# Optimization experiments

Measured on AMD Instinct MI355X. Metric: run time of the kernel, lower is better.

The kernel has to match this reference:

```python
import jax, jax.numpy as jnp
import numpy as np

N = 4096

def setup_inputs() -> dict:
    key = jax.random.key(0)
    kA, kB = jax.random.split(key)
    # A and B are upper-triangular inputs, as the module assumes
    A = jnp.triu(jax.random.normal(kA, (N, N), dtype=jnp.float32))
    B = jnp.triu(jax.random.normal(kB, (N, N), dtype=jnp.float32))
    return {"A": A, "B": B}

def reference(A, B):
    # C = triu(A @ B); product of upper-triangular matrices is upper-triangular,
    # the kernel additionally masks the lower triangle of the output.
    return jnp.triu(A @ B)
```

## Files before the change

kernel.cpp:

```cpp
#include <hip/hip_runtime.h>


#define N    4096
#define NB   32
#define BM   128
#define PK   64
#define NWG  1024
#define CH   12
#define MAXF 1280
#define MAXL 64

typedef __attribute__((ext_vector_type(8))) __bf16 bf16x8;
typedef __attribute__((ext_vector_type(4))) float  floatx4;
typedef __attribute__((ext_vector_type(8))) unsigned short ushort8;

struct Sched {
    unsigned short wgoff[NWG + 1];
    unsigned int   chunks[MAXF];
    int nf;
};

constexpr Sched make_sched() {
    Sched s{};
    unsigned int fr_sz[MAXF] = {};
    unsigned int fr_pk[MAXF] = {};
    int nf = 0;
    for (int d = NB - 1; d >= 0; --d) {
        const int npj  = 2 * (d + 1);
        const int nc   = (npj + CH - 1) / CH;
        const int base = npj / nc, rem = npj % nc;
        for (int bi = 0; bi + d < NB; ++bi) {
            const int bj = bi + d;
            int p0 = 0;
            for (int c = 0; c < nc; ++c) {
                const int fnp = base + (c < rem ? 1 : 0);
                fr_sz[nf] = (unsigned)fnp;
                fr_pk[nf] = (unsigned)bi | ((unsigned)bj << 5) |
                            ((unsigned)p0 << 10) | ((unsigned)fnp << 17) |
                            ((nc > 1 ? 1u : 0u) << 24);
                ++nf;
                p0 += fnp;
            }
        }
    }
    int order[MAXF] = {};
    int pos = 0;
    for (int sz = CH; sz >= 1; --sz)
        for (int i = 0; i < nf; ++i)
            if ((int)fr_sz[i] == sz) order[pos++] = i;
    int bcnt[MAXL] = {};
    int blist[MAXL][NWG] = {};
    for (int b = 0; b < NWG; ++b) blist[0][b] = NWG - 1 - b;
    bcnt[0] = NWG;
    int assign[MAXF] = {};
    int minload = 0;
    for (int k = 0; k < nf; ++k) {
        const int f = order[k];
        while (bcnt[minload] == 0) ++minload;
        const int b  = blist[minload][--bcnt[minload]];
        const int nl = minload + (int)fr_sz[f];
        blist[nl][bcnt[nl]++] = b;
        assign[f] = b;
    }
    int cnt[NWG] = {};
    for (int f = 0; f < nf; ++f) cnt[assign[f]]++;
    s.wgoff[0] = 0;
    for (int b = 0; b < NWG; ++b)
        s.wgoff[b + 1] = (unsigned short)(s.wgoff[b] + cnt[b]);
    int fill[NWG] = {};
    for (int f = 0; f < nf; ++f) {
        const int b = assign[f];
        s.chunks[s.wgoff[b] + fill[b]++] = fr_pk[f];
    }
    s.nf = nf;
    return s;
}

__device__ constexpr Sched g_sched = make_sched();

__device__ __forceinline__ unsigned short f32_to_bf16_rne(float f) {
    unsigned u = __builtin_bit_cast(unsigned, f);
    unsigned r = u + 0x7fffu + ((u >> 16) & 1u);
    return (unsigned short)(r >> 16);
}

__device__ __forceinline__ void gload_lds16(const unsigned short* g,
                                            unsigned short* l) {
    __builtin_amdgcn_global_load_lds(
        (const __attribute__((address_space(1))) void*)g,
        (__attribute__((address_space(3))) void*)l, 16, 0, 0);
}

__global__ __launch_bounds__(256)
void prep_kernel(const float* __restrict__ A, const float* __restrict__ B,
                 unsigned short* __restrict__ Ab, unsigned short* __restrict__ Bt,
                 float* __restrict__ C) {
    __shared__ float tile[64][65];
    const int bx = blockIdx.x, by = blockIdx.y;
    const int x0 = bx * 64, y0 = by * 64;
    const int xb = bx >> 1, yb = by >> 1;
    const int t  = threadIdx.x;
    const int tr = t >> 2, tc = (t & 3) * 16;

    if (xb >= yb) {
        const float* src = A + (size_t)(y0 + tr) * N + x0 + tc;
        const float4 v0 = ((const float4*)src)[0];
        const float4 v1 = ((const float4*)src)[1];
        const float4 v2 = ((const float4*)src)[2];
        const float4 v3 = ((const float4*)src)[3];
        ushort8 o0, o1;
        o0[0]=f32_to_bf16_rne(v0.x); o0[1]=f32_to_bf16_rne(v0.y);
        o0[2]=f32_to_bf16_rne(v0.z); o0[3]=f32_to_bf16_rne(v0.w);
        o0[4]=f32_to_bf16_rne(v1.x); o0[5]=f32_to_bf16_rne(v1.y);
        o0[6]=f32_to_bf16_rne(v1.z); o0[7]=f32_to_bf16_rne(v1.w);
        o1[0]=f32_to_bf16_rne(v2.x); o1[1]=f32_to_bf16_rne(v2.y);
        o1[2]=f32_to_bf16_rne(v2.z); o1[3]=f32_to_bf16_rne(v2.w);
        o1[4]=f32_to_bf16_rne(v3.x); o1[5]=f32_to_bf16_rne(v3.y);
        o1[6]=f32_to_bf16_rne(v3.z); o1[7]=f32_to_bf16_rne(v3.w);
        unsigned short* dst = Ab + (size_t)(y0 + tr) * N + x0 + tc;
        ((ushort8*)dst)[0] = o0;
        ((ushort8*)dst)[1] = o1;
    }
    if (xb <= yb) {
        const float* src = B + (size_t)(x0 + tr) * N + y0 + tc;
        const float4 v0 = ((const float4*)src)[0];
        const float4 v1 = ((const float4*)src)[1];
        const float4 v2 = ((const float4*)src)[2];
        const float4 v3 = ((const float4*)src)[3];
        float* d = &tile[tr][tc];
        d[0]=v0.x; d[1]=v0.y; d[2]=v0.z; d[3]=v0.w;
        d[4]=v1.x; d[5]=v1.y; d[6]=v1.z; d[7]=v1.w;
        d[8]=v2.x; d[9]=v2.y; d[10]=v2.z; d[11]=v2.w;
        d[12]=v3.x; d[13]=v3.y; d[14]=v3.z; d[15]=v3.w;
        __syncthreads();
        ushort8 o0, o1;
        #pragma unroll
        for (int i = 0; i < 8; ++i) o0[i] = f32_to_bf16_rne(tile[tc + i][tr]);
        #pragma unroll
        for (int i = 0; i < 8; ++i) o1[i] = f32_to_bf16_rne(tile[tc + 8 + i][tr]);
        unsigned short* dst = Bt + (size_t)(y0 + tr) * N + x0 + tc;
        ((ushort8*)dst)[0] = o0;
        ((ushort8*)dst)[1] = o1;
    }
    if (xb < yb || (xb - yb) >= 6) {
        float4 z = {0.f, 0.f, 0.f, 0.f};
        float* dst = C + (size_t)(y0 + tr) * N + x0 + tc;
        ((float4*)dst)[0] = z; ((float4*)dst)[1] = z;
        ((float4*)dst)[2] = z; ((float4*)dst)[3] = z;
    }
}

__global__ __launch_bounds__(256, 4)
void trimm_kernel(const unsigned short* __restrict__ Ab,
                  const unsigned short* __restrict__ Bt,
                  float* __restrict__ C) {
    __shared__ unsigned short sA[BM * PK];
    __shared__ unsigned short sB[BM * PK];

    const int tid  = threadIdx.x;
    const int w    = tid >> 6;
    const int lane = tid & 63;
    const int quad = lane >> 4;
    const int l15  = lane & 15;

    const int m0 = (w >> 1) * 64;
    const int n0 = (w & 1) * 64;

    const int srow   = lane >> 3;
    const int schunk = ((lane & 7) ^ srow) * 8;
    int rr[4];
    unsigned short* dA[4];
    unsigned short* dB[4];
    #pragma unroll
    for (int i = 0; i < 4; ++i) {
        rr[i] = w * 32 + i * 8 + srow;
        dA[i] = sA + (w * 32 + i * 8) * PK;
        dB[i] = sB + (w * 32 + i * 8) * PK;
    }

    const int e  = l15 & 7;
    const int c0 = ((quad ^ (e & 3)) + 4 * (e >> 2)) * 8;
    const int c1 = ((quad ^ (e & 3)) + 4 * (1 ^ (e >> 2))) * 8;

    const int b  = (int)blockIdx.x;
    const int j0 = g_sched.wgoff[b];
    const int j1 = g_sched.wgoff[b + 1];

    for (int j = j0; j < j1; ++j) {
        const unsigned int ck = g_sched.chunks[j];
        const int bi   = ck & 31;
        const int bj   = (ck >> 5) & 31;
        const int p0   = (ck >> 10) & 127;
        const int cnp  = (ck >> 17) & 127;
        const bool is_at = (ck >> 24) & 1u;

        const int row0 = bi * BM;
        const int col0 = bj * BM;
        const int k0   = bi * BM + p0 * PK;

        floatx4 acc[4][4] = {};

        const unsigned short* gA[4];
        const unsigned short* gB[4];
        #pragma unroll
        for (int i = 0; i < 4; ++i) {
            gA[i] = Ab + (size_t)(row0 + rr[i]) * N + k0 + schunk;
            gB[i] = Bt + (size_t)(col0 + rr[i]) * N + k0 + schunk;
        }

        for (int ph = 0; ph < cnp; ++ph) {
            #pragma unroll
            for (int i = 0; i < 4; ++i) { gload_lds16(gA[i], dA[i]); gA[i] += PK; }
            #pragma unroll
            for (int i = 0; i < 4; ++i) { gload_lds16(gB[i], dB[i]); gB[i] += PK; }
            __syncthreads();
            #pragma unroll
            for (int h = 0; h < 2; ++h) {
                const int ch = h ? c1 : c0;
                bf16x8 af[4], bfr[4];
                #pragma unroll
                for (int t = 0; t < 4; ++t) {
                    af[t]  = *(const bf16x8*)&sA[(m0 + t * 16 + l15) * PK + ch];
                    bfr[t] = *(const bf16x8*)&sB[(n0 + t * 16 + l15) * PK + ch];
                }
                #pragma unroll
                for (int tm = 0; tm < 4; ++tm)
                    #pragma unroll
                    for (int tn = 0; tn < 4; ++tn)
                        acc[tm][tn] = __builtin_amdgcn_mfma_f32_16x16x32_bf16(
                            af[tm], bfr[tn], acc[tm][tn], 0, 0, 0);
            }
            __syncthreads();
        }

        #pragma unroll
        for (int tm = 0; tm < 4; ++tm) {
            const int grow_base = row0 + m0 + tm * 16 + quad * 4;
            #pragma unroll
            for (int tn = 0; tn < 4; ++tn) {
                const int gcol = col0 + n0 + tn * 16 + l15;
                #pragma unroll
                for (int r = 0; r < 4; ++r) {
                    const int grow = grow_base + r;
                    const float v = acc[tm][tn][r];
                    if (is_at) {
                        atomicAdd(&C[(size_t)grow * N + gcol], v);
                    } else if (bi != bj) {
                        C[(size_t)grow * N + gcol] = v;
                    } else {
                        C[(size_t)grow * N + gcol] = (gcol >= grow) ? v : 0.0f;
                    }
                }
            }
        }
    }
}

extern "C" void kernel_launch(void* const* d_in, const int* in_sizes, int n_in,
                              void* d_out, int out_size, void* d_ws, size_t ws_size,
                              hipStream_t stream) {
    const float* A = (const float*)d_in[0];
    const float* B = (const float*)d_in[1];
    float* C = (float*)d_out;

    unsigned short* Ab = (unsigned short*)d_ws;
    unsigned short* Bt = Ab + (size_t)N * N;

    prep_kernel<<<dim3(N / 64, N / 64), dim3(256), 0, stream>>>(A, B, Ab, Bt, C);
    trimm_kernel<<<dim3(NWG), dim3(256), 0, stream>>>(Ab, Bt, C);
}
```

Before: 249.0 us.

## Double-buffer LDS tiles and halve workgroup count with larger chunks

Adds a two-stage LDS ping-pong so the global-to-LDS loads for the next K panel are issued before the MFMAs on the current panel run, removing one barrier per step. To fit the doubled shared memory, occupancy is lowered to 2 blocks per SIMD group. The persistent schedule is also changed to 512 workgroups with chunks of up to 24 panels, so atomic splitting happens on fewer, longer chunks, and the band in which C is pre-zeroed is widened to match. The cost is lower occupancy and fewer workgroups, which may leave some CUs idle or unbalanced.

```diff
diff --git a/kernel.cpp b/kernel.cpp
--- a/kernel.cpp
+++ b/kernel.cpp
@@ -5,9 +5,9 @@
 #define NB   32
 #define BM   128
 #define PK   64
-#define NWG  1024
-#define CH   12
-#define MAXF 1280
+#define NWG  512
+#define CH   24
+#define MAXF 832
 #define MAXL 64
 
 typedef __attribute__((ext_vector_type(8))) __bf16 bf16x8;
@@ -142,7 +142,7 @@
         ((ushort8*)dst)[0] = o0;
         ((ushort8*)dst)[1] = o1;
     }
-    if (xb < yb || (xb - yb) >= 6) {
+    if (xb < yb || (xb - yb) >= 12) {
         float4 z = {0.f, 0.f, 0.f, 0.f};
         float* dst = C + (size_t)(y0 + tr) * N + x0 + tc;
         ((float4*)dst)[0] = z; ((float4*)dst)[1] = z;
@@ -150,12 +150,12 @@
     }
 }
 
-__global__ __launch_bounds__(256, 4)
+__global__ __launch_bounds__(256, 2)
 void trimm_kernel(const unsigned short* __restrict__ Ab,
                   const unsigned short* __restrict__ Bt,
                   float* __restrict__ C) {
-    __shared__ unsigned short sA[BM * PK];
-    __shared__ unsigned short sB[BM * PK];
+    __shared__ unsigned short sA[2][BM * PK];
+    __shared__ unsigned short sB[2][BM * PK];
 
     const int tid  = threadIdx.x;
     const int w    = tid >> 6;
@@ -168,14 +168,11 @@
 
     const int srow   = lane >> 3;
     const int schunk = ((lane & 7) ^ srow) * 8;
-    int rr[4];
-    unsigned short* dA[4];
-    unsigned short* dB[4];
+    int rr[4], ldso[4];
     #pragma unroll
     for (int i = 0; i < 4; ++i) {
-        rr[i] = w * 32 + i * 8 + srow;
-        dA[i] = sA + (w * 32 + i * 8) * PK;
-        dB[i] = sB + (w * 32 + i * 8) * PK;
+        rr[i]   = w * 32 + i * 8 + srow;
+        ldso[i] = (w * 32 + i * 8) * PK;
     }
 
     const int e  = l15 & 7;
@@ -185,6 +182,8 @@
     const int b  = (int)blockIdx.x;
     const int j0 = g_sched.wgoff[b];
     const int j1 = g_sched.wgoff[b + 1];
+
+    int cur = 0;
 
     for (int j = j0; j < j1; ++j) {
         const unsigned int ck = g_sched.chunks[j];
@@ -208,20 +207,27 @@
             gB[i] = Bt + (size_t)(col0 + rr[i]) * N + k0 + schunk;
         }
 
-        for (int ph = 0; ph < cnp; ++ph) {
-            #pragma unroll
-            for (int i = 0; i < 4; ++i) { gload_lds16(gA[i], dA[i]); gA[i] += PK; }
-            #pragma unroll
-            for (int i = 0; i < 4; ++i) { gload_lds16(gB[i], dB[i]); gB[i] += PK; }
-            __syncthreads();
+        cur ^= 1;
+        #pragma unroll
+        for (int i = 0; i < 4; ++i) { gload_lds16(gA[i], &sA[cur][ldso[i]]); gA[i] += PK; }
+        #pragma unroll
+        for (int i = 0; i < 4; ++i) { gload_lds16(gB[i], &sB[cur][ldso[i]]); gB[i] += PK; }
+        __syncthreads();
+
+        for (int ph = 0; ph < cnp - 1; ++ph) {
+            const int nxt = cur ^ 1;
+            #pragma unroll
+            for (int i = 0; i < 4; ++i) { gload_lds16(gA[i], &sA[nxt][ldso[i]]); gA[i] += PK; }
+            #pragma unroll
+            for (int i = 0; i < 4; ++i) { gload_lds16(gB[i], &sB[nxt][ldso[i]]); gB[i] += PK; }
             #pragma unroll
             for (int h = 0; h < 2; ++h) {
                 const int ch = h ? c1 : c0;
                 bf16x8 af[4], bfr[4];
                 #pragma unroll
                 for (int t = 0; t < 4; ++t) {
-                    af[t]  = *(const bf16x8*)&sA[(m0 + t * 16 + l15) * PK + ch];
-                    bfr[t] = *(const bf16x8*)&sB[(n0 + t * 16 + l15) * PK + ch];
+                    af[t]  = *(const bf16x8*)&sA[cur][(m0 + t * 16 + l15) * PK + ch];
+                    bfr[t] = *(const bf16x8*)&sB[cur][(n0 + t * 16 + l15) * PK + ch];
                 }
                 #pragma unroll
                 for (int tm = 0; tm < 4; ++tm)
@@ -231,6 +237,25 @@
                             af[tm], bfr[tn], acc[tm][tn], 0, 0, 0);
             }
             __syncthreads();
+            cur = nxt;
+        }
+        {
+            #pragma unroll
+            for (int h = 0; h < 2; ++h) {
+                const int ch = h ? c1 : c0;
+                bf16x8 af[4], bfr[4];
+                #pragma unroll
+                for (int t = 0; t < 4; ++t) {
+                    af[t]  = *(const bf16x8*)&sA[cur][(m0 + t * 16 + l15) * PK + ch];
+                    bfr[t] = *(const bf16x8*)&sB[cur][(n0 + t * 16 + l15) * PK + ch];
+                }
+                #pragma unroll
+                for (int tm = 0; tm < 4; ++tm)
+                    #pragma unroll
+                    for (int tn = 0; tn < 4; ++tn)
+                        acc[tm][tn] = __builtin_amdgcn_mfma_f32_16x16x32_bf16(
+                            af[tm], bfr[tn], acc[tm][tn], 0, 0, 0);
+            }
         }
 
         #pragma unroll
```

Result: faster. 219.0 us (-12.1%).

## Software-pipeline triangular GEMM with register prefetch and double-buffered LDS across chunks

Applied to the files above, without the earlier changes.

Replaces the direct global-to-LDS loads with a register-staged prefetch that runs two k-phases ahead, continuing across chunk boundaries, into double-buffered LDS. This drops one barrier per phase and hides global latency behind MFMA work. Workgroups are halved to 512 with larger chunks (CH 24), and the zeroing range in the prep kernel is widened to match. The cost is more registers and twice the LDS, so occupancy is lowered to 2 blocks per SIMD via the launch bounds.

```diff
diff --git a/kernel.cpp b/kernel.cpp
--- a/kernel.cpp
+++ b/kernel.cpp
@@ -5,9 +5,9 @@
 #define NB   32
 #define BM   128
 #define PK   64
-#define NWG  1024
-#define CH   12
-#define MAXF 1280
+#define NWG  512
+#define CH   24
+#define MAXF 832
 #define MAXL 64
 
 typedef __attribute__((ext_vector_type(8))) __bf16 bf16x8;
@@ -84,13 +84,6 @@
     return (unsigned short)(r >> 16);
 }
 
-__device__ __forceinline__ void gload_lds16(const unsigned short* g,
-                                            unsigned short* l) {
-    __builtin_amdgcn_global_load_lds(
-        (const __attribute__((address_space(1))) void*)g,
-        (__attribute__((address_space(3))) void*)l, 16, 0, 0);
-}
-
 __global__ __launch_bounds__(256)
 void prep_kernel(const float* __restrict__ A, const float* __restrict__ B,
                  unsigned short* __restrict__ Ab, unsigned short* __restrict__ Bt,
@@ -142,7 +135,7 @@
         ((ushort8*)dst)[0] = o0;
         ((ushort8*)dst)[1] = o1;
     }
-    if (xb < yb || (xb - yb) >= 6) {
+    if (xb < yb || (xb - yb) >= 12) {
         float4 z = {0.f, 0.f, 0.f, 0.f};
         float* dst = C + (size_t)(y0 + tr) * N + x0 + tc;
         ((float4*)dst)[0] = z; ((float4*)dst)[1] = z;
@@ -150,12 +143,100 @@
     }
 }
 
-__global__ __launch_bounds__(256, 4)
+
+#define LA_DECODE() {                                                         \
+    const unsigned ck2 = g_sched.chunks[j2];                                  \
+    const int bi2 = ck2 & 31, bj2 = (ck2 >> 5) & 31;                          \
+    const int pp0 = (ck2 >> 10) & 127;                                        \
+    cnp2 = (ck2 >> 17) & 127;                                                 \
+    const int kk0 = bi2 * BM + pp0 * PK;                                      \
+    _Pragma("unroll")                                                         \
+    for (int i = 0; i < 4; ++i) {                                             \
+        la_a[i] = Ab + (size_t)(bi2 * BM + rr[i]) * N + kk0 + qlin;           \
+        la_b[i] = Bt + (size_t)(bj2 * BM + rr[i]) * N + kk0 + qlin;           \
+    }                                                                         \
+}
+
+#define LOAD_BANK(AB, BB)                                                     \
+    if (la_ok) {                                                              \
+        _Pragma("unroll")                                                     \
+        for (int i = 0; i < 4; ++i) AB[i] = *(const ushort8*)la_a[i];         \
+        _Pragma("unroll")                                                     \
+        for (int i = 0; i < 4; ++i) BB[i] = *(const ushort8*)la_b[i];         \
+        ++ph2;                                                                \
+        if (ph2 < cnp2) {                                                     \
+            _Pragma("unroll")                                                 \
+            for (int i = 0; i < 4; ++i) { la_a[i] += PK; la_b[i] += PK; }     \
+        } else {                                                              \
+            ++j2; ph2 = 0;                                                    \
+            if (j2 < j1) { LA_DECODE() } else { la_ok = false; }              \
+        }                                                                     \
+    }
+
+#define CD_DECODE() {                                                         \
+    const unsigned ckc = g_sched.chunks[j];                                   \
+    cbi = ckc & 31; cbj = (ckc >> 5) & 31;                                    \
+    cnp = (ckc >> 17) & 127;                                                  \
+    cat = (ckc >> 24) & 1u;                                                   \
+}
+
+#define EPILOGUE() {                                                          \
+    const int row0 = cbi * BM, col0 = cbj * BM;                               \
+    _Pragma("unroll")                                                         \
+    for (int tm = 0; tm < 4; ++tm) {                                          \
+        const int grow_base = row0 + m0 + tm * 16 + quad * 4;                 \
+        _Pragma("unroll")                                                     \
+        for (int tn = 0; tn < 4; ++tn) {                                      \
+            const int gcol = col0 + n0 + tn * 16 + l15;                       \
+            _Pragma("unroll")                                                 \
+            for (int r = 0; r < 4; ++r) {                                     \
+                const int grow = grow_base + r;                               \
+                const float v = acc[tm][tn][r];                               \
+                if (cat)            atomicAdd(&C[(size_t)grow * N + gcol], v);\
+                else if (cbi != cbj) C[(size_t)grow * N + gcol] = v;          \
+                else C[(size_t)grow * N + gcol] = (gcol >= grow) ? v : 0.0f;  \
+                acc[tm][tn][r] = 0.0f;                                        \
+            }                                                                 \
+        }                                                                     \
+    }                                                                         \
+}
+
+#define PHASE(B, AB, BB) {                                                    \
+    _Pragma("unroll")                                                         \
+    for (int i = 0; i < 4; ++i) *(ushort8*)&sA[B][lwofs[i]] = AB[i];          \
+    _Pragma("unroll")                                                         \
+    for (int i = 0; i < 4; ++i) *(ushort8*)&sB[B][lwofs[i]] = BB[i];          \
+    __syncthreads();                                                          \
+    LOAD_BANK(AB, BB)                                                         \
+    _Pragma("unroll")                                                         \
+    for (int h = 0; h < 2; ++h) {                                             \
+        const int chh = h ? c1 : c0;                                          \
+        bf16x8 af[4], bfr[4];                                                 \
+        _Pragma("unroll")                                                     \
+        for (int t = 0; t < 4; ++t) {                                         \
+            af[t]  = *(const bf16x8*)&sA[B][(m0 + t * 16 + l15) * PK + chh];  \
+            bfr[t] = *(const bf16x8*)&sB[B][(n0 + t * 16 + l15) * PK + chh];  \
+        }                                                                     \
+        _Pragma("unroll")                                                     \
+        for (int tm = 0; tm < 4; ++tm)                                        \
+            _Pragma("unroll")                                                 \
+            for (int tn = 0; tn < 4; ++tn)                                    \
+                acc[tm][tn] = __builtin_amdgcn_mfma_f32_16x16x32_bf16(        \
+                    af[tm], bfr[tn], acc[tm][tn], 0, 0, 0);                   \
+    }                                                                         \
+    if (++ph == cnp) {                                                        \
+        EPILOGUE()                                                            \
+        ++j; ph = 0;                                                          \
+        if (j < j1) CD_DECODE()                                               \
+    }                                                                         \
+}
+
+__global__ __launch_bounds__(256, 2)
 void trimm_kernel(const unsigned short* __restrict__ Ab,
                   const unsigned short* __restrict__ Bt,
                   float* __restrict__ C) {
-    __shared__ unsigned short sA[BM * PK];
-    __shared__ unsigned short sB[BM * PK];
+    __shared__ unsigned short sA[2][BM * PK];
+    __shared__ unsigned short sB[2][BM * PK];
 
     const int tid  = threadIdx.x;
     const int w    = tid >> 6;
@@ -166,16 +247,13 @@
     const int m0 = (w >> 1) * 64;
     const int n0 = (w & 1) * 64;
 
-    const int srow   = lane >> 3;
-    const int schunk = ((lane & 7) ^ srow) * 8;
-    int rr[4];
-    unsigned short* dA[4];
-    unsigned short* dB[4];
+    const int srow = lane >> 3;
+    const int qlin = (lane & 7) * 8;
+    int rr[4], lwofs[4];
     #pragma unroll
     for (int i = 0; i < 4; ++i) {
-        rr[i] = w * 32 + i * 8 + srow;
-        dA[i] = sA + (w * 32 + i * 8) * PK;
-        dB[i] = sB + (w * 32 + i * 8) * PK;
+        rr[i]    = w * 32 + i * 8 + srow;
+        lwofs[i] = rr[i] * PK + (((lane & 7) ^ srow) * 8);
     }
 
     const int e  = l15 & 7;
@@ -186,73 +264,27 @@
     const int j0 = g_sched.wgoff[b];
     const int j1 = g_sched.wgoff[b + 1];
 
-    for (int j = j0; j < j1; ++j) {
-        const unsigned int ck = g_sched.chunks[j];
-        const int bi   = ck & 31;
-        const int bj   = (ck >> 5) & 31;
-        const int p0   = (ck >> 10) & 127;
-        const int cnp  = (ck >> 17) & 127;
-        const bool is_at = (ck >> 24) & 1u;
-
-        const int row0 = bi * BM;
-        const int col0 = bj * BM;
-        const int k0   = bi * BM + p0 * PK;
-
-        floatx4 acc[4][4] = {};
-
-        const unsigned short* gA[4];
-        const unsigned short* gB[4];
-        #pragma unroll
-        for (int i = 0; i < 4; ++i) {
-            gA[i] = Ab + (size_t)(row0 + rr[i]) * N + k0 + schunk;
-            gB[i] = Bt + (size_t)(col0 + rr[i]) * N + k0 + schunk;
-        }
-
-        for (int ph = 0; ph < cnp; ++ph) {
-            #pragma unroll
-            for (int i = 0; i < 4; ++i) { gload_lds16(gA[i], dA[i]); gA[i] += PK; }
-            #pragma unroll
-            for (int i = 0; i < 4; ++i) { gload_lds16(gB[i], dB[i]); gB[i] += PK; }
-            __syncthreads();
-            #pragma unroll
-            for (int h = 0; h < 2; ++h) {
-                const int ch = h ? c1 : c0;
-                bf16x8 af[4], bfr[4];
-                #pragma unroll
-                for (int t = 0; t < 4; ++t) {
-                    af[t]  = *(const bf16x8*)&sA[(m0 + t * 16 + l15) * PK + ch];
-                    bfr[t] = *(const bf16x8*)&sB[(n0 + t * 16 + l15) * PK + ch];
-                }
-                #pragma unroll
-                for (int tm = 0; tm < 4; ++tm)
-                    #pragma unroll
-                    for (int tn = 0; tn < 4; ++tn)
-                        acc[tm][tn] = __builtin_amdgcn_mfma_f32_16x16x32_bf16(
-                            af[tm], bfr[tn], acc[tm][tn], 0, 0, 0);
-            }
-            __syncthreads();
-        }
-
-        #pragma unroll
-        for (int tm = 0; tm < 4; ++tm) {
-            const int grow_base = row0 + m0 + tm * 16 + quad * 4;
-            #pragma unroll
-            for (int tn = 0; tn < 4; ++tn) {
-                const int gcol = col0 + n0 + tn * 16 + l15;
-                #pragma unroll
-                for (int r = 0; r < 4; ++r) {
-                    const int grow = grow_base + r;
-                    const float v = acc[tm][tn][r];
-                    if (is_at) {
-                        atomicAdd(&C[(size_t)grow * N + gcol], v);
-                    } else if (bi != bj) {
-                        C[(size_t)grow * N + gcol] = v;
-                    } else {
-                        C[(size_t)grow * N + gcol] = (gcol >= grow) ? v : 0.0f;
-                    }
-                }
-            }
-        }
+    int  j = j0, ph = 0, cbi = 0, cbj = 0, cnp = 0;
+    bool cat = false;
+    if (j < j1) CD_DECODE()
+
+    int  j2 = j0, ph2 = 0, cnp2 = 0;
+    bool la_ok = (j2 < j1);
+    const unsigned short* la_a[4];
+    const unsigned short* la_b[4];
+    if (la_ok) LA_DECODE()
+
+    floatx4 acc[4][4] = {};
+    ushort8 aR0[4], bR0[4], aR1[4], bR1[4];
+
+    LOAD_BANK(aR0, bR0)
+    LOAD_BANK(aR1, bR1)
+
+    int par = 0;
+    while (j < j1) {
+        if (par == 0) { PHASE(0, aR0, bR0) }
+        else          { PHASE(1, aR1, bR1) }
+        par ^= 1;
     }
 }
 
```

After: 352.1 us. 41.4% more time.
